# Performance work log

Measured on AMD Instinct MI355X. Metric: run time of the kernel, lower is better.

The kernel has to match this reference:

```python
import jax, jax.numpy as jnp
import numpy as np
import math

D_MODEL = 512
N_HEAD = 8
TAU = 0.5


def _leaky_integrate(x):
    # dx/dt = -x / tau; x + dx/dt  (with tau=0.5 this equals -x)
    return x + (-x / TAU)


def setup_inputs() -> dict:
    key = jax.random.key(0)
    ks = jax.random.split(key, 12)
    B, S, D = 4, 2048, D_MODEL
    s = 1.0 / math.sqrt(D)
    inp = {
        "query": jax.random.normal(ks[0], (B, S, D), jnp.float32),
        "key": jax.random.normal(ks[1], (B, S, D), jnp.float32),
        "value": jax.random.normal(ks[2], (B, S, D), jnp.float32),
        "Wq": jax.random.normal(ks[3], (D, D), jnp.float32) * s,
        "bq": jnp.zeros((D,), jnp.float32),
        "Wk": jax.random.normal(ks[4], (D, D), jnp.float32) * s,
        "bk": jnp.zeros((D,), jnp.float32),
        "Wv": jax.random.normal(ks[5], (D, D), jnp.float32) * s,
        "bv": jnp.zeros((D,), jnp.float32),
        "Wo": jax.random.normal(ks[6], (D, D), jnp.float32) * s,
        "bo": jnp.zeros((D,), jnp.float32),
    }
    return inp


def reference(query, key, value, Wq, bq, Wk, bk, Wv, bv, Wo, bo):
    B, S, D = query.shape
    H = N_HEAD
    dh = D // H
    # linear projections (torch Linear: x @ W^T + b)
    q = query @ Wq.T + bq
    k = key @ Wk.T + bk
    v = value @ Wv.T + bv
    # (B, S, D) -> (B, H, S, dh)
    q = q.reshape(B, S, H, dh).transpose(0, 2, 1, 3)
    k = k.reshape(B, S, H, dh).transpose(0, 2, 1, 3)
    v = v.reshape(B, S, H, dh).transpose(0, 2, 1, 3)
    # leaky integration on q, k
    q = _leaky_integrate(q)
    k = _leaky_integrate(k)
    # scores scaled by sqrt(d_model) (NOT head dim) per the source
    scores = jnp.einsum("bhsd,bhtd->bhst", q, k) / math.sqrt(D_MODEL)
    attn = jax.nn.softmax(scores, axis=-1)
    # conductance-based synapse: elementwise sigmoid AFTER softmax
    attn = jax.nn.sigmoid(attn)
    out = jnp.einsum("bhst,bhtd->bhsd", attn, v)
    out = out.transpose(0, 2, 1, 3).reshape(B, S, D)
    return out @ Wo.T + bo
```

## Files before the change

### kernel.cpp

```cpp
#include <hip/hip_runtime.h>
#include <stdint.h>
#include <math.h>

using u16    = unsigned short;
using short8 = __attribute__((ext_vector_type(8))) short;
using f32x4  = __attribute__((ext_vector_type(4))) float;
using f32x16 = __attribute__((ext_vector_type(16))) float;
using u32x4  = __attribute__((ext_vector_type(4))) uint32_t;

#define DEVI __device__ __forceinline__
#define FENCE asm volatile("" ::: "memory")
#define GPTR(p) ((const __attribute__((address_space(1))) uint32_t*)(p))
#define LPTR(p) ((__attribute__((address_space(3))) uint32_t*)(p))

static constexpr int S  = 2048;
static constexpr int D  = 512;
static constexpr int DH = 64;
static constexpr float C2 = 0.063763906f;

DEVI u16 f2bf(float f){
  uint32_t u = __float_as_uint(f);
  u = u + 0x7FFFu + ((u >> 16) & 1u);
  return (u16)(u >> 16);
}

DEVI uint32_t cvt_pk_bf16(float a, float b){
  uint32_t d;
  asm("v_cvt_pk_bf16_f32 %0, %1, %2" : "=v"(d) : "v"(a), "v"(b));
  return d;
}

__global__ void k_cvtw(const float* __restrict__ a, const float* __restrict__ b,
                       const float* __restrict__ c, const float* __restrict__ d,
                       u16* __restrict__ out){
  int i = blockIdx.x * blockDim.x + threadIdx.x;
  int sel = i >> 16;
  const float* src = sel == 0 ? a : sel == 1 ? b : sel == 2 ? c : d;
  float4 v = reinterpret_cast<const float4*>(src)[i & ((1<<16)-1)];
  uint2 o;
  o.x = (uint32_t)f2bf(v.x) | ((uint32_t)f2bf(v.y) << 16);
  o.y = (uint32_t)f2bf(v.z) | ((uint32_t)f2bf(v.w) << 16);
  reinterpret_cast<uint2*>(out)[i] = o;
}

__global__ __launch_bounds__(512)
void k_gemm_qkv(const float* __restrict__ Xq, const float* __restrict__ Xk,
                const float* __restrict__ Xv, const u16* __restrict__ Wall,
                const float* __restrict__ bq, const float* __restrict__ bk,
                const float* __restrict__ bv,
                u16* __restrict__ Qp, u16* __restrict__ Kp, u16* __restrict__ Vtp)
{
  __shared__ __align__(16) u16 As[2][128*64];
  __shared__ __align__(16) u16 Bs[2][128*64];
  const int tid = threadIdx.x;
  const int w = tid >> 6, l = tid & 63;
  const int wm = w & 3, wn = w >> 2;
  const int m0 = blockIdx.x * 128, n0 = blockIdx.y * 128;
  const int z = blockIdx.z;
  const int srow = l >> 3, sslot = l & 7;

  const float* X = z == 0 ? Xq : (z == 1 ? Xk : Xv);
  const u16*   W = Wall + (size_t)z * 512 * 512;
  const float* bias = z == 0 ? bq : (z == 1 ? bk : bv);
  const float oscale = z == 0 ? C2 : 1.0f;

  const int arow = tid >> 2;
  const int ac   = (tid & 3) * 16;

  f32x4 acc[2][4];
  #pragma unroll
  for (int i = 0; i < 2; i++)
    #pragma unroll
    for (int j = 0; j < 4; j++)
      #pragma unroll
      for (int r = 0; r < 4; r++) acc[i][j][r] = 0.f;

  float4 av[2][4];
  auto LOADA = [&](int p, int kt){
    #pragma unroll
    for (int j = 0; j < 4; j++)
      av[p][j] = *reinterpret_cast<const float4*>(&X[(long)(m0 + arow)*D + kt + ac + j*4]);
  };
  auto WRITEA = [&](int buf, int p){
    #pragma unroll
    for (int j2 = 0; j2 < 2; j2++){
      u32x4 pkv;
      pkv[0] = cvt_pk_bf16(av[p][2*j2].x,   av[p][2*j2].y);
      pkv[1] = cvt_pk_bf16(av[p][2*j2].z,   av[p][2*j2].w);
      pkv[2] = cvt_pk_bf16(av[p][2*j2+1].x, av[p][2*j2+1].y);
      pkv[3] = cvt_pk_bf16(av[p][2*j2+1].z, av[p][2*j2+1].w);
      int slot = ((ac >> 3) + j2) ^ (arow & 7);
      *reinterpret_cast<u32x4*>(&As[buf][arow*64 + slot*8]) = pkv;
    }
  };
  auto STAGEB = [&](int buf, int kt){
    #pragma unroll
    for (int i = 0; i < 2; i++){
      int r = w*16 + i*8 + srow;
      int scol = (sslot ^ (r & 7)) * 8;
      __builtin_amdgcn_global_load_lds(GPTR(W + (long)(n0 + r)*D + kt + scol),
                                       LPTR(&Bs[buf][(w*16 + i*8)*64]), 16, 0, 0);
    }
  };

  LOADA(0, 0);
  STAGEB(0, 0);
  WRITEA(0, 0);
  LOADA(1, 64);
  asm volatile("s_waitcnt vmcnt(4) lgkmcnt(0)" ::: "memory");
  __builtin_amdgcn_s_barrier();
  FENCE;

  #pragma unroll
  for (int t = 0; t < 8; t++){
    const int buf = t & 1;
    if (t < 7) STAGEB(buf ^ 1, (t+1)*64);
    if (t < 6) LOADA(t & 1, (t+2)*64);
    #pragma unroll
    for (int ks = 0; ks < 2; ks++){
      short8 af[2];
      #pragma unroll
      for (int mf = 0; mf < 2; mf++){
        int row = wm*32 + mf*16 + (l & 15);
        int cw = (ks*4 + (l >> 4)) ^ (row & 7);
        af[mf] = *reinterpret_cast<const short8*>(&As[buf][(row*8 + cw)*8]);
      }
      #pragma unroll
      for (int nf = 0; nf < 4; nf++){
        int row = wn*64 + nf*16 + (l & 15);
        int cw = (ks*4 + (l >> 4)) ^ (row & 7);
        short8 bf = *reinterpret_cast<const short8*>(&Bs[buf][(row*8 + cw)*8]);
        #pragma unroll
        for (int mf = 0; mf < 2; mf++)
          acc[mf][nf] = __builtin_amdgcn_mfma_f32_16x16x32_bf16(af[mf], bf, acc[mf][nf], 0, 0, 0);
      }
    }
    if (t < 7) WRITEA(buf ^ 1, (t+1) & 1);
    if (t < 6)      asm volatile("s_waitcnt vmcnt(4) lgkmcnt(0)" ::: "memory");
    else if (t == 6) asm volatile("s_waitcnt vmcnt(0) lgkmcnt(0)" ::: "memory");
    if (t < 7){ __builtin_amdgcn_s_barrier(); FENCE; }
  }

  #pragma unroll
  for (int mf = 0; mf < 2; mf++){
    #pragma unroll
    for (int nf = 0; nf < 4; nf++){
      int n = n0 + wn*64 + nf*16 + (l & 15);
      float bi = bias[n];
      int h_ = n >> 6, d_ = n & 63;
      if (z == 2){
        int mb = m0 + wm*32 + mf*16 + (l >> 4)*4;
        int b_ = mb >> 11, s_ = mb & 2047;
        uint2 o;
        o.x = (uint32_t)f2bf(acc[mf][nf][0] + bi) | ((uint32_t)f2bf(acc[mf][nf][1] + bi) << 16);
        o.y = (uint32_t)f2bf(acc[mf][nf][2] + bi) | ((uint32_t)f2bf(acc[mf][nf][3] + bi) << 16);
        *reinterpret_cast<uint2*>(&Vtp[((long)((b_*8 + h_)*64 + d_))*2048 + s_]) = o;
      } else {
        u16* outp = z == 0 ? Qp : Kp;
        #pragma unroll
        for (int r = 0; r < 4; r++){
          int m = m0 + wm*32 + mf*16 + (l >> 4)*4 + r;
          int b_ = m >> 11, s_ = m & 2047;
          outp[((long)((b_*8 + h_)*2048 + s_))*64 + d_] = f2bf((acc[mf][nf][r] + bi)*oscale);
        }
      }
    }
  }
}

__global__ __launch_bounds__(512)
void k_gemm_ao(const u16* __restrict__ A, const u16* __restrict__ W,
               const float* __restrict__ bias2, float* __restrict__ outp)
{
  __shared__ __align__(16) u16 As[3][128*64];
  __shared__ __align__(16) u16 Bs[3][128*64];
  const int tid = threadIdx.x;
  const int w = tid >> 6, l = tid & 63;
  const int wm = w & 3, wn = w >> 2;
  const int m0 = blockIdx.x * 128, n0 = blockIdx.y * 128;
  const int srow = l >> 3, sslot = l & 7;

  f32x4 acc[2][4];
  #pragma unroll
  for (int i = 0; i < 2; i++)
    #pragma unroll
    for (int j = 0; j < 4; j++)
      #pragma unroll
      for (int r = 0; r < 4; r++) acc[i][j][r] = 0.f;

  auto STAGE = [&](int buf, int kt){
    #pragma unroll
    for (int i = 0; i < 2; i++){
      int r = w*16 + i*8 + srow;
      int scol = (sslot ^ (r & 7)) * 8;
      int m = m0 + r, k = kt + scol;
      long ga = ((long)(((m >> 11)*8 + (k >> 6))*2048 + (m & 2047)))*64 + (k & 63);
      __builtin_amdgcn_global_load_lds(GPTR(A + ga), LPTR(&As[buf][(w*16 + i*8)*64]), 16, 0, 0);
      long gb = (long)(n0 + r)*D + kt + scol;
      __builtin_amdgcn_global_load_lds(GPTR(W + gb), LPTR(&Bs[buf][(w*16 + i*8)*64]), 16, 0, 0);
    }
  };

  STAGE(0, 0); STAGE(1, 64);
  asm volatile("s_waitcnt vmcnt(4)" ::: "memory");
  __builtin_amdgcn_s_barrier();
  FENCE;

  #pragma unroll
  for (int t = 0; t < 8; t++){
    const int buf = t % 3;
    if (t + 2 < 8) STAGE((t + 2) % 3, (t + 2)*64);
    #pragma unroll
    for (int ks = 0; ks < 2; ks++){
      short8 af[2];
      #pragma unroll
      for (int mf = 0; mf < 2; mf++){
        int row = wm*32 + mf*16 + (l & 15);
        int cw = (ks*4 + (l >> 4)) ^ (row & 7);
        af[mf] = *reinterpret_cast<const short8*>(&As[buf][(row*8 + cw)*8]);
      }
      #pragma unroll
      for (int nf = 0; nf < 4; nf++){
        int row = wn*64 + nf*16 + (l & 15);
        int cw = (ks*4 + (l >> 4)) ^ (row & 7);
        short8 bf = *reinterpret_cast<const short8*>(&Bs[buf][(row*8 + cw)*8]);
        #pragma unroll
        for (int mf = 0; mf < 2; mf++)
          acc[mf][nf] = __builtin_amdgcn_mfma_f32_16x16x32_bf16(af[mf], bf, acc[mf][nf], 0, 0, 0);
      }
    }
    if (t < 7){
      if (t < 6) asm volatile("s_waitcnt vmcnt(4)" ::: "memory");
      else       asm volatile("s_waitcnt vmcnt(0)" ::: "memory");
      __builtin_amdgcn_s_barrier();
      FENCE;
    }
  }

  #pragma unroll
  for (int mf = 0; mf < 2; mf++)
    #pragma unroll
    for (int nf = 0; nf < 4; nf++){
      int n = n0 + wn*64 + nf*16 + (l & 15);
      float bi = bias2[(m0 >> 11)*512 + n];
      #pragma unroll
      for (int r = 0; r < 4; r++){
        int m = m0 + wm*32 + mf*16 + (l >> 4)*4 + r;
        outp[(long)m*D + n] = acc[mf][nf][r] + bi;
      }
    }
}

__global__ __launch_bounds__(256)
void k_sumv(const u16* __restrict__ Vt, float* __restrict__ SV){
  const int w = threadIdx.x >> 6, l = threadIdx.x & 63;
  const int row = blockIdx.x*4 + w;
  const u16* src = Vt + (long)row * S;
  float s = 0.f;
  #pragma unroll
  for (int j = 0; j < 4; j++){
    short8 v = *reinterpret_cast<const short8*>(&src[j*512 + l*8]);
    #pragma unroll
    for (int e = 0; e < 8; e++)
      s += __uint_as_float(((uint32_t)(u16)v[e]) << 16);
  }
  #pragma unroll
  for (int m = 1; m < 64; m <<= 1) s += __shfl_xor(s, m, 64);
  if (l == 0) SV[row] = s;
}

__global__ __launch_bounds__(256)
void k_bias2(const float* __restrict__ SV, const float* __restrict__ Wo,
             const float* __restrict__ bo, float* __restrict__ bias2){
  const int w = threadIdx.x >> 6, l = threadIdx.x & 63;
  const int idx = blockIdx.x*4 + w;
  const int b = idx >> 9, n = idx & 511;
  float dot = 0.f;
  #pragma unroll
  for (int j = 0; j < 2; j++){
    float4 wv = *reinterpret_cast<const float4*>(&Wo[(long)n*512 + l*8 + j*4]);
    float4 sv = *reinterpret_cast<const float4*>(&SV[b*512 + l*8 + j*4]);
    dot += wv.x*sv.x + wv.y*sv.y + wv.z*sv.z + wv.w*sv.w;
  }
  #pragma unroll
  for (int m = 1; m < 64; m <<= 1) dot += __shfl_xor(dot, m, 64);
  if (l == 0) bias2[idx] = bo[n] + 0.5f * dot;
}

__global__ __launch_bounds__(512, 2)
void k_flash(const u16* __restrict__ Qp, const u16* __restrict__ Kp,
             const u16* __restrict__ Vt, u16* __restrict__ AO)
{
  __shared__ __align__(16) u16 Ks[2][4][32*64];
  __shared__ __align__(16) u16 Vs[2][4][64*32];
  const int tid = threadIdx.x, w = tid >> 6, l = tid & 63;
  const int g = w >> 2, w4 = w & 3;
  const int bh = blockIdx.x & 31, qt = blockIdx.x >> 5;
  const u16* Qb = Qp + (long)bh * S * DH;
  const int hi = l >> 5, ln = l & 31;

  short8 qfr[2][4];
  #pragma unroll
  for (int qh = 0; qh < 2; qh++)
    #pragma unroll
    for (int c = 0; c < 4; c++){
      int row = qt*256 + w4*64 + qh*32 + ln;
      qfr[qh][c] = *reinterpret_cast<const short8*>(&Qb[(long)row*DH + c*16 + hi*8]);
    }

  int koff[4], voff[4];
  #pragma unroll
  for (int c = 0; c < 4; c++)
    koff[c] = ln*64 + (((2*c + hi) ^ ((ln ^ (ln >> 3)) & 7))*8);
  #pragma unroll
  for (int ch = 0; ch < 2; ch++)
    #pragma unroll
    for (int nf = 0; nf < 2; nf++){
      int row = nf*32 + ln;
      voff[ch*2 + nf] = row*32 + (((2*ch + hi) ^ ((row ^ (row >> 2)) & 3))*8);
    }

  const u16* kptr = Kp + (long)bh*S*DH + g*2048;
  const u16* vptr = Vt + (long)bh*DH*S + g*32;
  const int rK = w4*8 + (l >> 3), sK = l & 7;
  const int rV = w4*16 + (l >> 2), sV = l & 3;
  const long ksrc = (long)rK*64 + ((sK ^ ((rK ^ (rK >> 3)) & 7))*8);
  const long vsrc = (long)rV*S  + ((sV ^ ((rV ^ (rV >> 2)) & 3))*8);

  auto STAGE = [&](int buf){
    __builtin_amdgcn_global_load_lds(GPTR(kptr + ksrc), LPTR(&Ks[g][buf][w4*512]), 16, 0, 0);
    __builtin_amdgcn_global_load_lds(GPTR(vptr + vsrc), LPTR(&Vs[g][buf][w4*512]), 16, 0, 0);
    kptr += 4096;
    vptr += 64;
  };

  f32x16 zero16;
  #pragma unroll
  for (int r = 0; r < 16; r++) zero16[r] = 0.f;
  f32x16 oacc[2][2];
  #pragma unroll
  for (int qh = 0; qh < 2; qh++)
    #pragma unroll
    for (int j = 0; j < 2; j++)
      #pragma unroll
      for (int r = 0; r < 16; r++) oacc[qh][j][r] = 0.f;
  float lsum[2] = {0.f, 0.f};

  const u16* KB = &Ks[g][0][0];
  const u16* VB = &Vs[g][0][0];

  auto COMPUTE = [&](int buf){
    const u16* KT = KB + buf*2048;
    const u16* VT = VB + buf*2048;
    short8 kfr[4];
    #pragma unroll
    for (int c = 0; c < 4; c++)
      kfr[c] = *reinterpret_cast<const short8*>(KT + koff[c]);
    __builtin_amdgcn_s_setprio(1);
    f32x16 sacc[2];
    #pragma unroll
    for (int qh = 0; qh < 2; qh++){
      sacc[qh] = __builtin_amdgcn_mfma_f32_32x32x16_bf16(kfr[0], qfr[qh][0], zero16, 0, 0, 0);
      #pragma unroll
      for (int c = 1; c < 4; c++)
        sacc[qh] = __builtin_amdgcn_mfma_f32_32x32x16_bf16(kfr[c], qfr[qh][c], sacc[qh], 0, 0, 0);
    }
    __builtin_amdgcn_s_setprio(0);
    uint32_t pk[2][8];
    #pragma unroll
    for (int qh = 0; qh < 2; qh++)
      #pragma unroll
      for (int j = 0; j < 8; j++){
        float e0 = __builtin_amdgcn_exp2f(sacc[qh][2*j]);
        float e1 = __builtin_amdgcn_exp2f(sacc[qh][2*j+1]);
        lsum[qh] += e0 + e1;
        pk[qh][j] = cvt_pk_bf16(e0, e1);
      }
    #pragma unroll
    for (int ch = 0; ch < 2; ch++){
      short8 af[2];
      #pragma unroll
      for (int qh = 0; qh < 2; qh++){
        auto s1 = __builtin_amdgcn_permlane32_swap(pk[qh][ch*4+0], pk[qh][ch*4+2], false, false);
        auto s2 = __builtin_amdgcn_permlane32_swap(pk[qh][ch*4+1], pk[qh][ch*4+3], false, false);
        u32x4 avv = { (uint32_t)s1[0], (uint32_t)s2[0], (uint32_t)s1[1], (uint32_t)s2[1] };
        af[qh] = __builtin_bit_cast(short8, avv);
      }
      __builtin_amdgcn_s_setprio(1);
      #pragma unroll
      for (int nf = 0; nf < 2; nf++){
        short8 vfrag = *reinterpret_cast<const short8*>(VT + voff[ch*2 + nf]);
        #pragma unroll
        for (int qh = 0; qh < 2; qh++)
          oacc[qh][nf] = __builtin_amdgcn_mfma_f32_32x32x16_bf16(af[qh], vfrag, oacc[qh][nf], 0, 0, 0);
      }
      __builtin_amdgcn_s_setprio(0);
    }
  };

  STAGE(0); STAGE(1); STAGE(2);
  asm volatile("s_waitcnt vmcnt(4)" ::: "memory");
  __builtin_amdgcn_s_barrier();
  FENCE;

  for (int tp = 0; tp < 7; tp++){
    #pragma unroll
    for (int tt = 0; tt < 4; tt++){
      STAGE((tt + 3) & 3);
      COMPUTE(tt);
      asm volatile("s_waitcnt vmcnt(4)" ::: "memory");
      __builtin_amdgcn_s_barrier();
      FENCE;
    }
  }
  STAGE(3);
  COMPUTE(0);
  asm volatile("s_waitcnt vmcnt(4)" ::: "memory");
  __builtin_amdgcn_s_barrier(); FENCE;
  COMPUTE(1);
  asm volatile("s_waitcnt vmcnt(2)" ::: "memory");
  __builtin_amdgcn_s_barrier(); FENCE;
  COMPUTE(2);
  asm volatile("s_waitcnt vmcnt(0)" ::: "memory");
  __builtin_amdgcn_s_barrier(); FENCE;
  COMPUTE(3);

  __syncthreads();

  lsum[0] += __shfl_xor(lsum[0], 32, 64);
  lsum[1] += __shfl_xor(lsum[1], 32, 64);

  float* OB = (float*)Ks;
  float* LB = (float*)Vs;

  #pragma unroll
  for (int qh = 0; qh < 2; qh++){
    if (g == 1){
      #pragma unroll
      for (int r = 0; r < 16; r++){
        int qrow = (r & 3) + 8*(r >> 2) + 4*hi;
        #pragma unroll
        for (int nf = 0; nf < 2; nf++)
          OB[w4*2048 + qrow*64 + nf*32 + ln] = oacc[qh][nf][r];
      }
      if (hi == 0) LB[w4*32 + ln] = lsum[qh];
    }
    __syncthreads();
    if (g == 0){
      float lt = lsum[qh] + LB[w4*32 + ln];
      float linv = 0.25f / lt;
      #pragma unroll
      for (int r = 0; r < 16; r++){
        int qrow = (r & 3) + 8*(r >> 2) + 4*hi;
        float sc = __shfl(linv, qrow, 64);
        int s_ = qt*256 + w4*64 + qh*32 + qrow;
        #pragma unroll
        for (int nf = 0; nf < 2; nf++){
          float o = oacc[qh][nf][r] + OB[w4*2048 + qrow*64 + nf*32 + ln];
          AO[((long)bh*S + s_)*DH + nf*32 + ln] = f2bf(o * sc);
        }
      }
    }
    __syncthreads();
  }
}

extern "C" void kernel_launch(void* const* d_in, const int* in_sizes, int n_in,
                              void* d_out, int out_size, void* d_ws, size_t ws_size,
                              hipStream_t stream)
{
  const float* query = (const float*)d_in[0];
  const float* key_  = (const float*)d_in[1];
  const float* value = (const float*)d_in[2];
  const float* Wq = (const float*)d_in[3];
  const float* bq = (const float*)d_in[4];
  const float* Wk = (const float*)d_in[5];
  const float* bk = (const float*)d_in[6];
  const float* Wv = (const float*)d_in[7];
  const float* bv = (const float*)d_in[8];
  const float* Wo = (const float*)d_in[9];
  const float* bo = (const float*)d_in[10];

  char* ws = (char*)d_ws;
  const size_t XSZ = (size_t)8192 * 512 * 2;
  const size_t WSZ = (size_t)512 * 512 * 2;
  u16* AO  = (u16*)(ws);
  u16* wqb = (u16*)(ws + XSZ);
  u16* wob = (u16*)(ws + XSZ + 3*WSZ);
  u16* Qp  = (u16*)(ws + XSZ + 4*WSZ);
  u16* Kp  = (u16*)(ws + 2*XSZ + 4*WSZ);
  u16* Vtp = (u16*)(ws + 3*XSZ + 4*WSZ);
  float* SV    = (float*)(ws + 4*XSZ + 4*WSZ);
  float* bias2 = (float*)(ws + 4*XSZ + 4*WSZ + 8192);

  k_cvtw<<<(4<<16)/256, 256, 0, stream>>>(Wq, Wk, Wv, Wo, wqb);

  dim3 gq(64, 4, 3);
  k_gemm_qkv<<<gq, 512, 0, stream>>>(query, key_, value, wqb, bq, bk, bv, Qp, Kp, Vtp);

  k_sumv <<<512, 256, 0, stream>>>(Vtp, SV);
  k_bias2<<<512, 256, 0, stream>>>(SV, Wo, bo, bias2);

  k_flash<<<256, 512, 0, stream>>>(Qp, Kp, Vtp, AO);

  dim3 gg(64, 4);
  k_gemm_ao<<<gg, 512, 0, stream>>>(AO, wob, bias2, (float*)d_out);
}
```

Before: 90.09 us.

## Software-pipeline QK of next tile with softmax/PV of current tile

Splits the per-tile compute into QK, exp/pack and PV stages and issues the QK MFMAs for tile t+1 before the exp and PV work of tile t, using double-buffered score accumulators. LDS staging grows from 4 to 8 buffers per group so the next tile's K is resident while the current V is still in use. The goal is to overlap transcendental/permute work with matrix-core work. The cost is doubled LDS usage, which at 512 threads with launch bounds of 2 may cut occupancy, plus extra register pressure from the second accumulator set. The setprio hints are dropped and the row-sum reduction is rebalanced into a tree.

```diff
diff --git a/kernel.cpp b/kernel.cpp
--- a/kernel.cpp
+++ b/kernel.cpp
@@ -291,8 +291,8 @@
 void k_flash(const u16* __restrict__ Qp, const u16* __restrict__ Kp,
              const u16* __restrict__ Vt, u16* __restrict__ AO)
 {
-  __shared__ __align__(16) u16 Ks[2][4][32*64];
-  __shared__ __align__(16) u16 Vs[2][4][64*32];
+  __shared__ __align__(16) u16 Ks[2][8][32*64];
+  __shared__ __align__(16) u16 Vs[2][8][64*32];
   const int tid = threadIdx.x, w = tid >> 6, l = tid & 63;
   const int g = w >> 2, w4 = w & 3;
   const int bh = blockIdx.x & 31, qt = blockIdx.x >> 5;
@@ -349,15 +349,15 @@
   const u16* KB = &Ks[g][0][0];
   const u16* VB = &Vs[g][0][0];
 
-  auto COMPUTE = [&](int buf){
+  f32x16 saccA[2], saccB[2];
+  short8 paf[2][2];
+
+  auto QK = [&](int buf, f32x16* sacc){
     const u16* KT = KB + buf*2048;
-    const u16* VT = VB + buf*2048;
     short8 kfr[4];
     #pragma unroll
     for (int c = 0; c < 4; c++)
       kfr[c] = *reinterpret_cast<const short8*>(KT + koff[c]);
-    __builtin_amdgcn_s_setprio(1);
-    f32x16 sacc[2];
     #pragma unroll
     for (int qh = 0; qh < 2; qh++){
       sacc[qh] = __builtin_amdgcn_mfma_f32_32x32x16_bf16(kfr[0], qfr[qh][0], zero16, 0, 0, 0);
@@ -365,65 +365,69 @@
       for (int c = 1; c < 4; c++)
         sacc[qh] = __builtin_amdgcn_mfma_f32_32x32x16_bf16(kfr[c], qfr[qh][c], sacc[qh], 0, 0, 0);
     }
-    __builtin_amdgcn_s_setprio(0);
-    uint32_t pk[2][8];
-    #pragma unroll
-    for (int qh = 0; qh < 2; qh++)
-      #pragma unroll
-      for (int j = 0; j < 8; j++){
-        float e0 = __builtin_amdgcn_exp2f(sacc[qh][2*j]);
-        float e1 = __builtin_amdgcn_exp2f(sacc[qh][2*j+1]);
-        lsum[qh] += e0 + e1;
-        pk[qh][j] = cvt_pk_bf16(e0, e1);
-      }
-    #pragma unroll
-    for (int ch = 0; ch < 2; ch++){
-      short8 af[2];
-      #pragma unroll
-      for (int qh = 0; qh < 2; qh++){
-        auto s1 = __builtin_amdgcn_permlane32_swap(pk[qh][ch*4+0], pk[qh][ch*4+2], false, false);
-        auto s2 = __builtin_amdgcn_permlane32_swap(pk[qh][ch*4+1], pk[qh][ch*4+3], false, false);
+  };
+  auto EXPPACK = [&](f32x16* sacc){
+    #pragma unroll
+    for (int qh = 0; qh < 2; qh++){
+      float e[16];
+      #pragma unroll
+      for (int j = 0; j < 16; j++) e[j] = __builtin_amdgcn_exp2f(sacc[qh][j]);
+      float s01 = (e[0]+e[1]) + (e[2]+e[3]);
+      float s23 = (e[4]+e[5]) + (e[6]+e[7]);
+      float s45 = (e[8]+e[9]) + (e[10]+e[11]);
+      float s67 = (e[12]+e[13]) + (e[14]+e[15]);
+      lsum[qh] += (s01 + s23) + (s45 + s67);
+      uint32_t pk[8];
+      #pragma unroll
+      for (int j = 0; j < 8; j++) pk[j] = cvt_pk_bf16(e[2*j], e[2*j+1]);
+      #pragma unroll
+      for (int ch = 0; ch < 2; ch++){
+        auto s1 = __builtin_amdgcn_permlane32_swap(pk[ch*4+0], pk[ch*4+2], false, false);
+        auto s2 = __builtin_amdgcn_permlane32_swap(pk[ch*4+1], pk[ch*4+3], false, false);
         u32x4 avv = { (uint32_t)s1[0], (uint32_t)s2[0], (uint32_t)s1[1], (uint32_t)s2[1] };
-        af[qh] = __builtin_bit_cast(short8, avv);
-      }
-      __builtin_amdgcn_s_setprio(1);
+        paf[ch][qh] = __builtin_bit_cast(short8, avv);
+      }
+    }
+  };
+  auto PV = [&](int buf){
+    const u16* VT = VB + buf*2048;
+    #pragma unroll
+    for (int ch = 0; ch < 2; ch++)
       #pragma unroll
       for (int nf = 0; nf < 2; nf++){
         short8 vfrag = *reinterpret_cast<const short8*>(VT + voff[ch*2 + nf]);
         #pragma unroll
         for (int qh = 0; qh < 2; qh++)
-          oacc[qh][nf] = __builtin_amdgcn_mfma_f32_32x32x16_bf16(af[qh], vfrag, oacc[qh][nf], 0, 0, 0);
-      }
-      __builtin_amdgcn_s_setprio(0);
-    }
+          oacc[qh][nf] = __builtin_amdgcn_mfma_f32_32x32x16_bf16(paf[ch][qh], vfrag, oacc[qh][nf], 0, 0, 0);
+      }
   };
 
   STAGE(0); STAGE(1); STAGE(2);
   asm volatile("s_waitcnt vmcnt(4)" ::: "memory");
   __builtin_amdgcn_s_barrier();
   FENCE;
-
-  for (int tp = 0; tp < 7; tp++){
-    #pragma unroll
-    for (int tt = 0; tt < 4; tt++){
-      STAGE((tt + 3) & 3);
-      COMPUTE(tt);
-      asm volatile("s_waitcnt vmcnt(4)" ::: "memory");
-      __builtin_amdgcn_s_barrier();
-      FENCE;
-    }
-  }
-  STAGE(3);
-  COMPUTE(0);
-  asm volatile("s_waitcnt vmcnt(4)" ::: "memory");
-  __builtin_amdgcn_s_barrier(); FENCE;
-  COMPUTE(1);
-  asm volatile("s_waitcnt vmcnt(2)" ::: "memory");
-  __builtin_amdgcn_s_barrier(); FENCE;
-  COMPUTE(2);
-  asm volatile("s_waitcnt vmcnt(0)" ::: "memory");
-  __builtin_amdgcn_s_barrier(); FENCE;
-  COMPUTE(3);
+  QK(0, saccA);
+
+  #pragma unroll 1
+  for (int tp = 0; tp < 4; tp++){
+    #pragma unroll
+    for (int tt = 0; tt < 8; tt++){
+      int t = tp*8 + tt;
+      if (t + 3 < 32) STAGE((tt + 3) & 7);
+      if (t < 29)      asm volatile("s_waitcnt vmcnt(4)" ::: "memory");
+      else if (t == 29) asm volatile("s_waitcnt vmcnt(2)" ::: "memory");
+      else if (t == 30) asm volatile("s_waitcnt vmcnt(0)" ::: "memory");
+      if (t < 31){ __builtin_amdgcn_s_barrier(); FENCE; }
+      if (tt & 1){
+        if (t < 31) QK((tt + 1) & 7, saccA);
+        EXPPACK(saccB);
+      } else {
+        if (t < 31) QK((tt + 1) & 7, saccB);
+        EXPPACK(saccA);
+      }
+      PV(tt);
+    }
+  }
 
   __syncthreads();
 
```

After: 184.1 us. +104.4%, slower.
